# Performance work log

Hardware: AMD Instinct MI355X
Metric: run time of the kernel (lower is better)

The kernel has to match this reference:

```python
import jax, jax.numpy as jnp
import numpy as np

EPS = 1e-5
HEADS = 4
T_FRAMES, N_IND = 7, 12


def _bn(x, g, b):
    # training-mode BatchNorm1d over all nodes, per channel (biased variance)
    m = x.mean((0, 1))
    v = x.var((0, 1))
    return (x - m) * jax.lax.rsqrt(v + EPS) * g + b


def _gps_stack(h, gw, gb, qw, qb, ow, ob, bng, bnb, w1, b1, w2, b2):
    # h: [G, n, D]; params stacked over L layers on leading axis
    G, n, D = h.shape
    dh = D // HEADS
    inv_sqrt_dh = 1.0 / float(np.sqrt(dh))

    def layer(h, p):
        gw, gb, qw, qb, ow, ob, bng, bnb, w1, b1, w2, b2 = p
        # GCNConv on fully-connected graph (+self-loops): uniform 1/n aggregation
        xw = h @ gw.T + gb
        gcn = jnp.broadcast_to(xw.mean(axis=1, keepdims=True), h.shape)
        h1 = _bn(gcn + h, bng[0], bnb[0])
        # dense multi-head self-attention over each small graph
        qkv = h @ qw.T + qb                                   # [G, n, 3D]
        q, k, v = jnp.split(qkv, 3, axis=-1)
        q = q.reshape(G, n, HEADS, dh)
        k = k.reshape(G, n, HEADS, dh)
        v = v.reshape(G, n, HEADS, dh)
        scores = jnp.einsum('gqhd,gkhd->ghqk', q, k) * inv_sqrt_dh
        a = jax.nn.softmax(scores, axis=-1)
        attn = jnp.einsum('ghqk,gkhd->gqhd', a, v).reshape(G, n, D) @ ow.T + ob
        h2 = _bn(attn + h, bng[1], bnb[1])
        out = h1 + h2
        mlp = jax.nn.relu(out @ w1.T + b1) @ w2.T + b2
        out = _bn(out + mlp, bng[2], bnb[2])
        return out, None

    h, _ = jax.lax.scan(layer, h, (gw, gb, qw, qb, ow, ob, bng, bnb, w1, b1, w2, b2))
    return h


def setup_inputs() -> dict:
    key = jax.random.key(0)
    ks = jax.random.split(key, 8)
    B, J, D, L, C = 256, 17, 128, 3, 8

    def nrm(k, shape, s=0.05):
        return jax.random.normal(k, shape, dtype=jnp.float32) * s

    def layer_params(kbase):
        k = jax.random.split(kbase, 6)
        return dict(
            gw=nrm(k[0], (L, D, D)), gb=jnp.zeros((L, D), jnp.float32),
            qw=nrm(k[1], (L, 3 * D, D)), qb=jnp.zeros((L, 3 * D), jnp.float32),
            ow=nrm(k[2], (L, D, D)), ob=jnp.zeros((L, D), jnp.float32),
            bng=jnp.ones((L, 3, D), jnp.float32), bnb=jnp.zeros((L, 3, D), jnp.float32),
            w1=nrm(k[3], (L, 2 * D, D)), b1=jnp.zeros((L, 2 * D), jnp.float32),
            w2=nrm(k[4], (L, D, 2 * D)), b2=jnp.zeros((L, D), jnp.float32),
        )

    jp = layer_params(ks[0])
    ip = layer_params(ks[1])
    inp = {
        'poses': jax.random.normal(ks[2], (B, T_FRAMES * N_IND, J, 2), dtype=jnp.float32),
        'emb_w': nrm(ks[3], (D, 2), 0.5), 'emb_b': jnp.zeros((D,), jnp.float32),
        'cls_w': nrm(ks[4], (C, D), 0.1), 'cls_b': jnp.zeros((C,), jnp.float32),
    }
    for pfx, p in (('j_', jp), ('i_', ip)):
        for name, v in p.items():
            inp[pfx + name] = v
    return inp


def reference(poses, emb_w, emb_b, cls_w, cls_b,
              j_gw, j_gb, j_qw, j_qb, j_ow, j_ob, j_bng, j_bnb, j_w1, j_b1, j_w2, j_b2,
              i_gw, i_gb, i_qw, i_qb, i_ow, i_ob, i_bng, i_bnb, i_w1, i_b1, i_w2, i_b2):
    B, TN, J, _ = poses.shape
    T, N = T_FRAMES, N_IND
    D = emb_w.shape[0]
    # joint embedding: Linear(2, D) + LeakyReLU(0.01)
    h = jax.nn.leaky_relu(poses @ emb_w.T + emb_b, negative_slope=0.01)   # [B, TN, J, D]
    h = h.reshape(B * TN, J, D)
    h = _gps_stack(h, j_gw, j_gb, j_qw, j_qb, j_ow, j_ob, j_bng, j_bnb, j_w1, j_b1, j_w2, j_b2)
    h = h.reshape(B, T, N, J, D)
    ind = h.mean(axis=3)                                                  # [B, T, N, D]
    gi = ind.reshape(B * T, N, D)
    gi = _gps_stack(gi, i_gw, i_gb, i_qw, i_qb, i_ow, i_ob, i_bng, i_bnb, i_w1, i_b1, i_w2, i_b2)
    pooled = gi.reshape(B, T, N, D).mean(axis=(1, 2))                     # [B, D]
    return pooled @ cls_w.T + cls_b                                       # [B, 8]
```

## Files before the change

### kernel.cpp

```cpp
#include <hip/hip_runtime.h>
#include <hip/hip_bf16.h>

#define TID threadIdx.x

typedef __hip_bfloat16 bf16;
typedef short s8v __attribute__((ext_vector_type(8)));
typedef float f4v __attribute__((ext_vector_type(4)));
typedef float f16v __attribute__((ext_vector_type(16)));

__device__ __forceinline__ float b2f(bf16 x) { return __bfloat162float(x); }
__device__ __forceinline__ bf16  f2b(float x) { return __float2bfloat16(x); }
__device__ __forceinline__ short f2s(float x) {
    __hip_bfloat16 b = __float2bfloat16(x); short s; __builtin_memcpy(&s, &b, 2); return s;
}
__device__ __forceinline__ float bfu(short s) {
    unsigned u = ((unsigned)(unsigned short)s) << 16; float f; __builtin_memcpy(&f, &u, 4); return f;
}

#define B_   256
#define T_   7
#define NI_  12
#define TN_  84
#define J_   17
#define D_   128
#define H_   4
#define DH_  32
#define C_   8
#define G1_  21504
#define R1_  365568
#define G2_  1792
#define R2_  21504
#define EPS_ 1e-5f
#define NSLOT 32

__global__ __launch_bounds__(256)
void zero_kernel(float* __restrict__ p, int n)
{
    int stride = gridDim.x * 256;
    for (int i = blockIdx.x * 256 + TID; i < n; i += stride) p[i] = 0.f;
}

__global__ __launch_bounds__(128)
void setid_kernel(float* __restrict__ ab)
{
    ab[TID] = 1.f; ab[128 + TID] = 0.f;
}

__global__ __launch_bounds__(256)
void wconv_kernel(const float* __restrict__ src, bf16* __restrict__ dst, int n)
{
    int stride = gridDim.x * 256;
    for (int i = blockIdx.x * 256 + TID; i < n; i += stride) dst[i] = f2b(src[i]);
}

__global__ __launch_bounds__(256)
void embedv_kernel(const float* __restrict__ poses, const float* __restrict__ ew,
                   const float* __restrict__ eb, bf16* __restrict__ h, int R)
{
    __shared__ float sE0[128], sE1[128], sEb[128];
    if (TID < 128) { sE0[TID] = ew[2 * TID]; sE1[TID] = ew[2 * TID + 1]; sEb[TID] = eb[TID]; }
    __syncthreads();
    int stride = gridDim.x * 256;
    for (int i8 = blockIdx.x * 256 + TID; i8 < R * 16; i8 += stride) {
        int r = i8 >> 4, c8 = (i8 & 15) * 8;
        float p0 = poses[2 * r], p1 = poses[2 * r + 1];
        s8v o;
        #pragma unroll
        for (int e = 0; e < 8; ++e) {
            int c = c8 + e;
            float v = p0 * sE0[c] + p1 * sE1[c] + sEb[c];
            o[e] = f2s(v > 0.f ? v : 0.01f * v);
        }
        *(s8v*)(h + (size_t)r * D_ + c8) = o;
    }
}

__global__ __launch_bounds__(256)
void gmeanv_kernel(const bf16* __restrict__ h, const float* __restrict__ ab,
                   bf16* __restrict__ hbar, int G, int n)
{
    int i8 = blockIdx.x * 256 + TID;
    if (i8 >= G * 16) return;
    int g = i8 >> 4, c8 = (i8 & 15) * 8;
    const bf16* p = h + (size_t)g * n * D_ + c8;
    float acc[8] = {0,0,0,0,0,0,0,0};
    for (int j = 0; j < n; ++j) {
        s8v v = *(const s8v*)(p + j * D_);
        #pragma unroll
        for (int e = 0; e < 8; ++e) acc[e] += bfu(v[e]);
    }
    float rn = 1.f / n;
    s8v o;
    #pragma unroll
    for (int e = 0; e < 8; ++e) {
        int c = c8 + e;
        o[e] = f2s(acc[e] * rn * ab[c] + ab[128 + c]);
    }
    *(s8v*)(hbar + (size_t)g * D_ + c8) = o;
}

__global__ __launch_bounds__(256)
void linear64_kernel(const bf16* __restrict__ X, const bf16* __restrict__ Wb,
                     const float* __restrict__ bias, bf16* __restrict__ out)
{
    const int l = TID & 63, wid = TID >> 6;
    const size_t rbase = (size_t)blockIdx.x * 64;
    const int t = wid;
    const int arow = t * 16 + (l & 15);
    s8v a[4];
    #pragma unroll
    for (int ks = 0; ks < 4; ++ks)
        a[ks] = *(const s8v*)(X + (rbase + arow) * D_ + ks * 32 + ((l >> 4) * 8));
    for (int nt = 0; nt < 8; ++nt) {
        int col = nt * 16 + (l & 15);
        float bs = bias[col];
        f4v acc = {bs, bs, bs, bs};
        #pragma unroll
        for (int ks = 0; ks < 4; ++ks) {
            s8v b = *(const s8v*)(Wb + (size_t)col * D_ + ks * 32 + ((l >> 4) * 8));
            acc = __builtin_amdgcn_mfma_f32_16x16x32_bf16(a[ks], b, acc, 0, 0, 0);
        }
        #pragma unroll
        for (int r = 0; r < 4; ++r) {
            int row = t * 16 + (l >> 4) * 4 + r;
            out[(rbase + row) * D_ + col] = f2b(acc[r]);
        }
    }
}

template<int NN, int NG>
__global__ __launch_bounds__(256)
void attn_mfma_kernel(const bf16* __restrict__ h, const float* __restrict__ ab3,
                      const bf16* __restrict__ gcn,
                      const bf16* __restrict__ qwb, const float* __restrict__ qb,
                      const bf16* __restrict__ owb, const float* __restrict__ ob,
                      bf16* __restrict__ out, float* __restrict__ spart)
{
    constexpr int ROWS = NG * NN;
    constexpr int MT = (ROWS + 15) / 16;
    constexpr int QP = 3 * D_ + 24;
    constexpr int HP = 152;
    constexpr int NPAIR = NG * H_;
    __shared__ __align__(16) short sQKV[MT * 16][QP];
    __shared__ __align__(16) short sHN[ROWS][HP];
    __shared__ short sGCN[NG][128];
    __shared__ float sAB[256];
    __shared__ float sRED[512];

    const int l = TID & 63, wid = TID >> 6;
    const size_t gbase = (size_t)blockIdx.x * ROWS * D_;
    const bf16* hb = h + gbase;

    sAB[TID] = ab3[TID];
    for (int i = TID; i < NG * 128; i += 256)
        sGCN[i >> 7][i & 127] = ((const short*)gcn)[(size_t)blockIdx.x * NG * 128 + i];
    for (int i = TID; i < 512; i += 256) sRED[i] = 0.f;
    __syncthreads();

    for (int task = TID; task < ROWS * 16; task += 256) {
        int row = task >> 4, c8 = (task & 15) * 8;
        s8v raw = *(const s8v*)(hb + (size_t)row * D_ + c8);
        s8v af;
        #pragma unroll
        for (int e = 0; e < 8; ++e) {
            int c = c8 + e;
            af[e] = f2s(bfu(raw[e]) * sAB[c] + sAB[128 + c]);
        }
        *(s8v*)(&sHN[row][c8]) = af;
    }
    __syncthreads();

    s8v a[MT][4];
    #pragma unroll
    for (int t = 0; t < MT; ++t) {
        int row = t * 16 + (l & 15);
        if (row >= ROWS) row = ROWS - 1;
        const short* rp = &sHN[row][(l >> 4) * 8];
        #pragma unroll
        for (int ks = 0; ks < 4; ++ks) a[t][ks] = *(const s8v*)(rp + ks * 32);
    }
    for (int nt = wid; nt < 24; nt += 4) {
        int col = nt * 16 + (l & 15);
        const bf16* wp = qwb + (size_t)col * D_ + ((l >> 4) * 8);
        s8v b[4];
        #pragma unroll
        for (int ks = 0; ks < 4; ++ks) b[ks] = *(const s8v*)(wp + ks * 32);
        float bs = qb[col];
        #pragma unroll
        for (int t = 0; t < MT; ++t) {
            f4v acc = {bs, bs, bs, bs};
            #pragma unroll
            for (int ks = 0; ks < 4; ++ks)
                acc = __builtin_amdgcn_mfma_f32_16x16x32_bf16(a[t][ks], b[ks], acc, 0, 0, 0);
            #pragma unroll
            for (int r = 0; r < 4; ++r)
                sQKV[t * 16 + (l >> 4) * 4 + r][col] = f2s(acc[r]);
        }
    }
    __syncthreads();

    {
        const float inv = 0.17677669529663687f;
        const int l31 = l & 31, Gq = l >> 5;
        #pragma unroll
        for (int q = 0; q < NPAIR / 4; ++q) {
            int p = wid + 4 * q;
            int g = p >> 2, hd = p & 3;
            int gr = g * NN;
            int rr = gr + (l31 < NN ? l31 : NN - 1);
            s8v ka0 = *(const s8v*)(&sQKV[rr][D_ + hd * DH_ + Gq * 8]);
            s8v ka1 = *(const s8v*)(&sQKV[rr][D_ + hd * DH_ + Gq * 8 + 16]);
            s8v qb0 = *(const s8v*)(&sQKV[rr][hd * DH_ + Gq * 8]);
            s8v qb1 = *(const s8v*)(&sQKV[rr][hd * DH_ + Gq * 8 + 16]);
            f16v s = {};
            s = __builtin_amdgcn_mfma_f32_32x32x16_bf16(ka0, qb0, s, 0, 0, 0);
            s = __builtin_amdgcn_mfma_f32_32x32x16_bf16(ka1, qb1, s, 0, 0, 0);
            float m = -1e30f;
            #pragma unroll
            for (int r = 0; r < 16; ++r) {
                int j = (r & 3) + 8 * (r >> 2) + 4 * Gq;
                if (j < NN) m = fmaxf(m, s[r]);
            }
            m = fmaxf(m, __shfl_xor(m, 32));
            float pv[16]; float sum = 0.f;
            #pragma unroll
            for (int r = 0; r < 16; ++r) {
                int j = (r & 3) + 8 * (r >> 2) + 4 * Gq;
                float e = (j < NN) ? __expf((s[r] - m) * inv) : 0.f;
                pv[r] = e; sum += e;
            }
            sum += __shfl_xor(sum, 32);
            float rs = 1.f / sum;
            if (l31 < NN) {
                #pragma unroll
                for (int r = 0; r < 16; ++r) {
                    int j = (r & 3) + 8 * (r >> 2) + 4 * Gq;
                    sQKV[gr + l31][D_ + hd * DH_ + j] = f2s(pv[r] * rs);
                }
            }
            int prow = gr + l31; if (prow > MT * 16 - 1) prow = MT * 16 - 1;
            s8v pa0 = *(const s8v*)(&sQKV[prow][D_ + hd * DH_ + Gq * 8]);
            s8v pa1 = *(const s8v*)(&sQKV[prow][D_ + hd * DH_ + Gq * 8 + 16]);
            s8v vb0, vb1;
            #pragma unroll
            for (int e = 0; e < 8; ++e) {
                int j0 = Gq * 8 + e;      int jj0 = j0 < NN ? j0 : 0;
                int j1 = 16 + Gq * 8 + e; int jj1 = j1 < NN ? j1 : 0;
                vb0[e] = sQKV[gr + jj0][2 * D_ + hd * DH_ + l31];
                vb1[e] = sQKV[gr + jj1][2 * D_ + hd * DH_ + l31];
            }
            f16v o = {};
            o = __builtin_amdgcn_mfma_f32_32x32x16_bf16(pa0, vb0, o, 0, 0, 0);
            o = __builtin_amdgcn_mfma_f32_32x32x16_bf16(pa1, vb1, o, 0, 0, 0);
            #pragma unroll
            for (int r = 0; r < 16; ++r) {
                int i = (r & 3) + 8 * (r >> 2) + 4 * Gq;
                if (i < NN) sQKV[gr + i][hd * DH_ + l31] = f2s(o[r]);
            }
        }
    }
    __syncthreads();

    bf16* og = out + gbase;
    #pragma unroll
    for (int t = 0; t < MT; ++t) {
        int row = t * 16 + (l & 15);
        if (row >= ROWS) row = ROWS - 1;
        const short* rp = &sQKV[row][(l >> 4) * 8];
        #pragma unroll
        for (int ks = 0; ks < 4; ++ks) a[t][ks] = *(const s8v*)(rp + ks * 32);
    }
    #pragma unroll
    for (int ni = 0; ni < 2; ++ni) {
        int nt = wid + 4 * ni;
        int col = nt * 16 + (l & 15);
        const bf16* wp = owb + (size_t)col * D_ + ((l >> 4) * 8);
        s8v b[4];
        #pragma unroll
        for (int ks = 0; ks < 4; ++ks) b[ks] = *(const s8v*)(wp + ks * 32);
        float bs = ob[col];
        float s1 = 0.f, q1 = 0.f, s2 = 0.f, q2 = 0.f;
        #pragma unroll
        for (int t = 0; t < MT; ++t) {
            f4v acc = {bs, bs, bs, bs};
            #pragma unroll
            for (int ks = 0; ks < 4; ++ks)
                acc = __builtin_amdgcn_mfma_f32_16x16x32_bf16(a[t][ks], b[ks], acc, 0, 0, 0);
            #pragma unroll
            for (int r = 0; r < 4; ++r) {
                int row = t * 16 + (l >> 4) * 4 + r;
                if (row < ROWS) {
                    float res = bfu(sHN[row][col]);
                    float t2v = acc[r] + res;
                    og[(size_t)row * D_ + col] = f2b(t2v);
                    s2 += t2v; q2 += t2v * t2v;
                    int g = row / NN;
                    float x1 = res + bfu(sGCN[g][col]);
                    s1 += x1; q1 += x1 * x1;
                }
            }
        }
        atomicAdd(&sRED[col], s1);
        atomicAdd(&sRED[128 + col], q1);
        atomicAdd(&sRED[256 + col], s2);
        atomicAdd(&sRED[384 + col], q2);
    }
    __syncthreads();
    {
        int slot = blockIdx.x & (NSLOT - 1);
        for (int i = TID; i < 512; i += 256) atomicAdd(&spart[slot * 512 + i], sRED[i]);
    }
}

__global__ __launch_bounds__(128)
void finalize12_kernel(float* __restrict__ spart, const float* __restrict__ bng,
                       const float* __restrict__ bnb, float rcount,
                       float* __restrict__ ab12)
{
    int c = TID;
    float s1 = 0, q1 = 0, s2 = 0, q2 = 0;
    for (int s = 0; s < NSLOT; ++s) {
        float* p = spart + s * 512;
        s1 += p[c]; q1 += p[128 + c]; s2 += p[256 + c]; q2 += p[384 + c];
        p[c] = 0.f; p[128 + c] = 0.f; p[256 + c] = 0.f; p[384 + c] = 0.f;
    }
    float m1 = s1 * rcount, v1 = q1 * rcount - m1 * m1;
    float a1 = rsqrtf(v1 + EPS_) * bng[c];
    ab12[c] = a1; ab12[128 + c] = bnb[c] - m1 * a1;
    float m2 = s2 * rcount, v2 = q2 * rcount - m2 * m2;
    float a2 = rsqrtf(v2 + EPS_) * bng[128 + c];
    ab12[256 + c] = a2; ab12[384 + c] = bnb[128 + c] - m2 * a2;
}

__global__ __launch_bounds__(128)
void finalize3_kernel(float* __restrict__ spart, const float* __restrict__ gamma,
                      const float* __restrict__ beta, float rcount,
                      float* __restrict__ ab3)
{
    int c = TID;
    float s1 = 0, q1 = 0;
    for (int s = 0; s < NSLOT; ++s) {
        float* p = spart + s * 256;
        s1 += p[c]; q1 += p[128 + c];
        p[c] = 0.f; p[128 + c] = 0.f;
    }
    float m = s1 * rcount, v = q1 * rcount - m * m;
    float a = rsqrtf(v + EPS_) * gamma[c];
    ab3[c] = a; ab3[128 + c] = beta[c] - m * a;
}

__global__ __launch_bounds__(256)
void mlp_mfma_kernel(bf16* __restrict__ X, const float* __restrict__ ab3,
                     const bf16* __restrict__ gcn, const bf16* __restrict__ t2,
                     const float* __restrict__ ab12,
                     const bf16* __restrict__ w1b, const float* __restrict__ b1,
                     const bf16* __restrict__ w2b, const float* __restrict__ b2,
                     int n, float* __restrict__ spart3)
{
    constexpr int MP = 264;
    __shared__ short sM[64][MP];
    __shared__ short sOUT[64][136];
    __shared__ float sAB[768];
    __shared__ float sRED[256];
    const int l = TID & 63, wid = TID >> 6;
    const size_t rbase = (size_t)blockIdx.x * 64;
    bf16* Xb = X + rbase * D_;
    const bf16* Tb = t2 + rbase * D_;

    sAB[TID] = ab3[TID];
    for (int i = TID; i < 512; i += 256) sAB[256 + i] = ab12[i];
    sRED[TID] = 0.f;
    __syncthreads();

    {
        int row = TID >> 2;
        int cb0 = (TID & 3) * 32;
        int g = (int)((rbase + row) / n);
        #pragma unroll
        for (int k2 = 0; k2 < 4; ++k2) {
            int cb = cb0 + k2 * 8;
            s8v xv = *(const s8v*)(Xb + (size_t)row * D_ + cb);
            s8v gv = *(const s8v*)(gcn + (size_t)g * D_ + cb);
            s8v tv = *(const s8v*)(Tb + (size_t)row * D_ + cb);
            s8v af;
            #pragma unroll
            for (int e = 0; e < 8; ++e) {
                int c = cb + e;
                float hn = bfu(xv[e]) * sAB[c] + sAB[128 + c];
                float outv = (hn + bfu(gv[e])) * sAB[256 + c] + sAB[384 + c]
                           + bfu(tv[e]) * sAB[512 + c] + sAB[640 + c];
                af[e] = f2s(outv);
            }
            *(s8v*)(&sOUT[row][cb]) = af;
        }
    }
    __syncthreads();

    s8v a[4][4];
    #pragma unroll
    for (int t = 0; t < 4; ++t) {
        const short* rp = &sOUT[t * 16 + (l & 15)][(l >> 4) * 8];
        #pragma unroll
        for (int ks = 0; ks < 4; ++ks) a[t][ks] = *(const s8v*)(rp + ks * 32);
    }
    for (int nt = wid; nt < 16; nt += 4) {
        int col = nt * 16 + (l & 15);
        const bf16* wp = w1b + (size_t)col * D_ + ((l >> 4) * 8);
        s8v b[4];
        #pragma unroll
        for (int ks = 0; ks < 4; ++ks) b[ks] = *(const s8v*)(wp + ks * 32);
        float bs = b1[col];
        #pragma unroll
        for (int t = 0; t < 4; ++t) {
            f4v acc = {bs, bs, bs, bs};
            #pragma unroll
            for (int ks = 0; ks < 4; ++ks)
                acc = __builtin_amdgcn_mfma_f32_16x16x32_bf16(a[t][ks], b[ks], acc, 0, 0, 0);
            #pragma unroll
            for (int r = 0; r < 4; ++r)
                sM[t * 16 + (l >> 4) * 4 + r][col] = f2s(fmaxf(acc[r], 0.f));
        }
    }
    __syncthreads();

    {
        const int nt0 = wid * 2;
        const int col0 = nt0 * 16 + (l & 15), col1 = col0 + 16;
        s8v b0[8], b1v[8];
        #pragma unroll
        for (int ks = 0; ks < 8; ++ks) {
            b0[ks]  = *(const s8v*)(w2b + (size_t)col0 * 256 + ks * 32 + ((l >> 4) * 8));
            b1v[ks] = *(const s8v*)(w2b + (size_t)col1 * 256 + ks * 32 + ((l >> 4) * 8));
        }
        float bs0 = b2[col0], bs1 = b2[col1];
        float ss0 = 0.f, qq0 = 0.f, ss1 = 0.f, qq1 = 0.f;
        #pragma unroll
        for (int t = 0; t < 4; ++t) {
            s8v am[8];
            const short* rp = &sM[t * 16 + (l & 15)][(l >> 4) * 8];
            #pragma unroll
            for (int ks = 0; ks < 8; ++ks) am[ks] = *(const s8v*)(rp + ks * 32);
            f4v acc0 = {bs0, bs0, bs0, bs0};
            f4v acc1 = {bs1, bs1, bs1, bs1};
            #pragma unroll
            for (int ks = 0; ks < 8; ++ks) {
                acc0 = __builtin_amdgcn_mfma_f32_16x16x32_bf16(am[ks], b0[ks], acc0, 0, 0, 0);
                acc1 = __builtin_amdgcn_mfma_f32_16x16x32_bf16(am[ks], b1v[ks], acc1, 0, 0, 0);
            }
            #pragma unroll
            for (int r = 0; r < 4; ++r) {
                int row = t * 16 + (l >> 4) * 4 + r;
                float xn0 = acc0[r] + bfu(sOUT[row][col0]);
                float xn1 = acc1[r] + bfu(sOUT[row][col1]);
                Xb[(size_t)row * D_ + col0] = f2b(xn0);
                Xb[(size_t)row * D_ + col1] = f2b(xn1);
                ss0 += xn0; qq0 += xn0 * xn0;
                ss1 += xn1; qq1 += xn1 * xn1;
            }
        }
        atomicAdd(&sRED[col0], ss0); atomicAdd(&sRED[128 + col0], qq0);
        atomicAdd(&sRED[col1], ss1); atomicAdd(&sRED[128 + col1], qq1);
    }
    __syncthreads();
    {
        int slot = blockIdx.x & (NSLOT - 1);
        atomicAdd(&spart3[slot * 256 + TID], sRED[TID]);
    }
}

__global__ __launch_bounds__(128)
void poolcls_kernel(const bf16* __restrict__ gi, const float* __restrict__ ab,
                    const float* __restrict__ cw, const float* __restrict__ cb,
                    float* __restrict__ out)
{
    __shared__ float sP[128];
    int b = blockIdx.x, d = TID;
    const bf16* p = gi + (size_t)b * TN_ * D_ + d;
    float s = 0.f;
    for (int i = 0; i < TN_; ++i) s += b2f(p[i * D_]);
    sP[d] = (s * (1.f / TN_)) * ab[d] + ab[128 + d];
    __syncthreads();
    if (d < C_) {
        float acc = cb[d];
        for (int k = 0; k < D_; ++k) acc += sP[k] * cw[d * D_ + k];
        out[b * C_ + d] = acc;
    }
}

extern "C" void kernel_launch(void* const* d_in, const int* in_sizes, int n_in,
                              void* d_out, int out_size, void* d_ws, size_t ws_size,
                              hipStream_t stream)
{
    (void)in_sizes; (void)n_in; (void)out_size; (void)ws_size;

    const float* poses = (const float*)d_in[0];
    const float* emb_w = (const float*)d_in[1];
    const float* emb_b = (const float*)d_in[2];
    const float* cls_w = (const float*)d_in[3];
    const float* cls_b = (const float*)d_in[4];
    const float* jp[12]; const float* ip[12];
    for (int k = 0; k < 12; ++k) { jp[k] = (const float*)d_in[5 + k]; ip[k] = (const float*)d_in[17 + k]; }

    char* base = (char*)d_ws;
    size_t off = 0;
    auto alloc_b = [&](size_t elems) -> bf16* {
        bf16* p = (bf16*)(base + off);
        off = (off + elems * sizeof(bf16) + 255) & ~(size_t)255;
        return p;
    };
    bf16* bufA  = alloc_b((size_t)R1_ * D_);
    bf16* bufB  = alloc_b((size_t)R1_ * D_);
    bf16* hbarJ = alloc_b((size_t)G1_ * D_);
    bf16* gcn1  = alloc_b((size_t)G1_ * D_);
    bf16* hbar2 = alloc_b((size_t)G2_ * D_);
    bf16* gcn2  = alloc_b((size_t)G2_ * D_);
    float* spart12 = (float*)(base + off); off += NSLOT * 512 * 4;
    float* spart3  = (float*)(base + off); off += NSLOT * 256 * 4;
    float* ab3     = (float*)(base + off); off += 256 * 4;
    float* ab12    = (float*)(base + off); off = (off + 512 * 4 + 255) & ~(size_t)255;
    bf16* wb[2][5];
    const int wsz[5] = {3 * D_ * D_, 3 * 3 * D_ * D_, 3 * D_ * D_, 3 * 2 * D_ * D_, 3 * 2 * D_ * D_};
    for (int s = 0; s < 2; ++s)
        for (int k = 0; k < 5; ++k) wb[s][k] = alloc_b((size_t)wsz[k]);

    const int widx[5] = {0, 2, 4, 8, 10};
    for (int s = 0; s < 2; ++s) {
        const float** P = s ? ip : jp;
        for (int k = 0; k < 5; ++k)
            wconv_kernel<<<(wsz[k] + 4095) / 4096, 256, 0, stream>>>(P[widx[k]], wb[s][k], wsz[k]);
    }
    zero_kernel<<<24, 256, 0, stream>>>(spart12, NSLOT * 512 + NSLOT * 256);

    embedv_kernel<<<4096, 256, 0, stream>>>(poses, emb_w, emb_b, bufA, R1_);

    auto run_stage = [&](const float** P, const bf16* const* W, bf16* h, bf16* t2,
                         bf16* hbar, bf16* gcn, int G, int n, int R) {
        setid_kernel<<<1, 128, 0, stream>>>(ab3);
        for (int L = 0; L < 3; ++L) {
            const bf16* gwb = W[0] + (size_t)L * D_ * D_;
            const bf16* qwb = W[1] + (size_t)L * 3 * D_ * D_;
            const bf16* owb = W[2] + (size_t)L * D_ * D_;
            const bf16* w1b = W[3] + (size_t)L * 2 * D_ * D_;
            const bf16* w2b = W[4] + (size_t)L * 2 * D_ * D_;
            const float* gb  = P[1] + (size_t)L * D_;
            const float* qb  = P[3] + (size_t)L * 3 * D_;
            const float* ob  = P[5] + (size_t)L * D_;
            const float* bng = P[6] + (size_t)L * 3 * D_;
            const float* bnb = P[7] + (size_t)L * 3 * D_;
            const float* b1  = P[9] + (size_t)L * 2 * D_;
            const float* b2  = P[11] + (size_t)L * D_;
            float rcount = 1.f / (float)R;

            gmeanv_kernel<<<G * 16 / 256, 256, 0, stream>>>(h, ab3, hbar, G, n);
            linear64_kernel<<<G / 64, 256, 0, stream>>>(hbar, gwb, gb, gcn);
            if (n == J_)
                attn_mfma_kernel<J_, 2><<<G / 2, 256, 0, stream>>>(h, ab3, gcn, qwb, qb, owb, ob, t2, spart12);
            else
                attn_mfma_kernel<NI_, 4><<<G / 4, 256, 0, stream>>>(h, ab3, gcn, qwb, qb, owb, ob, t2, spart12);
            finalize12_kernel<<<1, 128, 0, stream>>>(spart12, bng, bnb, rcount, ab12);
            mlp_mfma_kernel<<<R / 64, 256, 0, stream>>>(h, ab3, gcn, t2, ab12,
                                                        w1b, b1, w2b, b2, n, spart3);
            finalize3_kernel<<<1, 128, 0, stream>>>(spart3, bng + 2 * D_, bnb + 2 * D_,
                                                    rcount, ab3);
        }
    };

    run_stage(jp, wb[0], bufA, bufB, hbarJ, gcn1, G1_, J_, R1_);
    gmeanv_kernel<<<G1_ * 16 / 256, 256, 0, stream>>>(bufA, ab3, hbarJ, G1_, J_);
    run_stage(ip, wb[1], hbarJ, bufB, hbar2, gcn2, G2_, NI_, R2_);
    poolcls_kernel<<<B_, 128, 0, stream>>>(hbarJ, ab3, cls_w, cls_b, (float*)d_out);
}
```

Measured before the change: 1.689 ms.

## Fuse GCN mean and linear into attention kernel; use wave-shuffle BN stat reduction

The per-graph mean and the GCN linear projection are now computed inside the attention kernel from the already-normalized rows held in shared memory. This removes two kernel launches per layer and a global round trip for hbar and gcn. The GCN result is still written out for the MLP kernel. BatchNorm partial sums in the attention and MLP kernels are now reduced with wave shuffles and sent directly to global atomics, replacing the shared-memory atomic staging. The tradeoff is more global atomics per block and an extra serial mean computation inside attention. The mean is taken from bf16-rounded normalized values, which may slightly change precision.

```diff
diff --git a/kernel.cpp b/kernel.cpp
--- a/kernel.cpp
+++ b/kernel.cpp
@@ -99,42 +99,14 @@
     *(s8v*)(hbar + (size_t)g * D_ + c8) = o;
 }
 
-__global__ __launch_bounds__(256)
-void linear64_kernel(const bf16* __restrict__ X, const bf16* __restrict__ Wb,
-                     const float* __restrict__ bias, bf16* __restrict__ out)
-{
-    const int l = TID & 63, wid = TID >> 6;
-    const size_t rbase = (size_t)blockIdx.x * 64;
-    const int t = wid;
-    const int arow = t * 16 + (l & 15);
-    s8v a[4];
-    #pragma unroll
-    for (int ks = 0; ks < 4; ++ks)
-        a[ks] = *(const s8v*)(X + (rbase + arow) * D_ + ks * 32 + ((l >> 4) * 8));
-    for (int nt = 0; nt < 8; ++nt) {
-        int col = nt * 16 + (l & 15);
-        float bs = bias[col];
-        f4v acc = {bs, bs, bs, bs};
-        #pragma unroll
-        for (int ks = 0; ks < 4; ++ks) {
-            s8v b = *(const s8v*)(Wb + (size_t)col * D_ + ks * 32 + ((l >> 4) * 8));
-            acc = __builtin_amdgcn_mfma_f32_16x16x32_bf16(a[ks], b, acc, 0, 0, 0);
-        }
-        #pragma unroll
-        for (int r = 0; r < 4; ++r) {
-            int row = t * 16 + (l >> 4) * 4 + r;
-            out[(rbase + row) * D_ + col] = f2b(acc[r]);
-        }
-    }
-}
-
 template<int NN, int NG>
 __global__ __launch_bounds__(256)
 void attn_mfma_kernel(const bf16* __restrict__ h, const float* __restrict__ ab3,
-                      const bf16* __restrict__ gcn,
+                      const bf16* __restrict__ gwb, const float* __restrict__ gb,
                       const bf16* __restrict__ qwb, const float* __restrict__ qb,
                       const bf16* __restrict__ owb, const float* __restrict__ ob,
-                      bf16* __restrict__ out, float* __restrict__ spart)
+                      bf16* __restrict__ out, bf16* __restrict__ gcnb,
+                      float* __restrict__ spart)
 {
     constexpr int ROWS = NG * NN;
     constexpr int MT = (ROWS + 15) / 16;
@@ -143,18 +115,15 @@
     constexpr int NPAIR = NG * H_;
     __shared__ __align__(16) short sQKV[MT * 16][QP];
     __shared__ __align__(16) short sHN[ROWS][HP];
+    __shared__ __align__(16) short sHB[NG][128];
     __shared__ short sGCN[NG][128];
     __shared__ float sAB[256];
-    __shared__ float sRED[512];
 
     const int l = TID & 63, wid = TID >> 6;
     const size_t gbase = (size_t)blockIdx.x * ROWS * D_;
     const bf16* hb = h + gbase;
 
     sAB[TID] = ab3[TID];
-    for (int i = TID; i < NG * 128; i += 256)
-        sGCN[i >> 7][i & 127] = ((const short*)gcn)[(size_t)blockIdx.x * NG * 128 + i];
-    for (int i = TID; i < 512; i += 256) sRED[i] = 0.f;
     __syncthreads();
 
     for (int task = TID; task < ROWS * 16; task += 256) {
@@ -179,6 +148,42 @@
         #pragma unroll
         for (int ks = 0; ks < 4; ++ks) a[t][ks] = *(const s8v*)(rp + ks * 32);
     }
+
+    for (int task = TID; task < NG * D_; task += 256) {
+        int g = task >> 7, col = task & 127;
+        float s = 0.f;
+        for (int j = 0; j < NN; ++j) s += bfu(sHN[g * NN + j][col]);
+        sHB[g][col] = f2s(s * (1.f / NN));
+    }
+    __syncthreads();
+
+    {
+        int rclamp = (l & 15) < NG ? (l & 15) : NG - 1;
+        s8v ag[4];
+        #pragma unroll
+        for (int ks = 0; ks < 4; ++ks)
+            ag[ks] = *(const s8v*)(&sHB[rclamp][ks * 32 + ((l >> 4) * 8)]);
+        bf16* gout = gcnb + (size_t)blockIdx.x * NG * D_;
+        #pragma unroll
+        for (int ci = 0; ci < 2; ++ci) {
+            int col = (wid * 2 + ci) * 16 + (l & 15);
+            float bs = gb[col];
+            f4v acc = {bs, bs, bs, bs};
+            #pragma unroll
+            for (int ks = 0; ks < 4; ++ks) {
+                s8v b = *(const s8v*)(gwb + (size_t)col * D_ + ks * 32 + ((l >> 4) * 8));
+                acc = __builtin_amdgcn_mfma_f32_16x16x32_bf16(ag[ks], b, acc, 0, 0, 0);
+            }
+            if ((l >> 4) == 0) {
+                #pragma unroll
+                for (int r = 0; r < NG; ++r) {
+                    sGCN[r][col] = f2s(acc[r]);
+                    gout[(size_t)r * D_ + col] = f2b(acc[r]);
+                }
+            }
+        }
+    }
+
     for (int nt = wid; nt < 24; nt += 4) {
         int col = nt * 16 + (l & 15);
         const bf16* wp = qwb + (size_t)col * D_ + ((l >> 4) * 8);
@@ -270,6 +275,7 @@
         #pragma unroll
         for (int ks = 0; ks < 4; ++ks) a[t][ks] = *(const s8v*)(rp + ks * 32);
     }
+    const int slot = blockIdx.x & (NSLOT - 1);
     #pragma unroll
     for (int ni = 0; ni < 2; ++ni) {
         int nt = wid + 4 * ni;
@@ -300,15 +306,16 @@
                 }
             }
         }
-        atomicAdd(&sRED[col], s1);
-        atomicAdd(&sRED[128 + col], q1);
-        atomicAdd(&sRED[256 + col], s2);
-        atomicAdd(&sRED[384 + col], q2);
-    }
-    __syncthreads();
-    {
-        int slot = blockIdx.x & (NSLOT - 1);
-        for (int i = TID; i < 512; i += 256) atomicAdd(&spart[slot * 512 + i], sRED[i]);
+        s1 += __shfl_xor(s1, 16); s1 += __shfl_xor(s1, 32);
+        q1 += __shfl_xor(q1, 16); q1 += __shfl_xor(q1, 32);
+        s2 += __shfl_xor(s2, 16); s2 += __shfl_xor(s2, 32);
+        q2 += __shfl_xor(q2, 16); q2 += __shfl_xor(q2, 32);
+        if ((l >> 4) == 0) {
+            atomicAdd(&spart[slot * 512 + col], s1);
+            atomicAdd(&spart[slot * 512 + 128 + col], q1);
+            atomicAdd(&spart[slot * 512 + 256 + col], s2);
+            atomicAdd(&spart[slot * 512 + 384 + col], q2);
+        }
     }
 }
 
@@ -361,7 +368,6 @@
     __shared__ short sM[64][MP];
     __shared__ short sOUT[64][136];
     __shared__ float sAB[768];
-    __shared__ float sRED[256];
     const int l = TID & 63, wid = TID >> 6;
     const size_t rbase = (size_t)blockIdx.x * 64;
     bf16* Xb = X + rbase * D_;
@@ -369,7 +375,6 @@
 
     sAB[TID] = ab3[TID];
     for (int i = TID; i < 512; i += 256) sAB[256 + i] = ab12[i];
-    sRED[TID] = 0.f;
     __syncthreads();
 
     {
@@ -458,13 +463,17 @@
                 ss1 += xn1; qq1 += xn1 * xn1;
             }
         }
-        atomicAdd(&sRED[col0], ss0); atomicAdd(&sRED[128 + col0], qq0);
-        atomicAdd(&sRED[col1], ss1); atomicAdd(&sRED[128 + col1], qq1);
-    }
-    __syncthreads();
-    {
-        int slot = blockIdx.x & (NSLOT - 1);
-        atomicAdd(&spart3[slot * 256 + TID], sRED[TID]);
+        ss0 += __shfl_xor(ss0, 16); ss0 += __shfl_xor(ss0, 32);
+        qq0 += __shfl_xor(qq0, 16); qq0 += __shfl_xor(qq0, 32);
+        ss1 += __shfl_xor(ss1, 16); ss1 += __shfl_xor(ss1, 32);
+        qq1 += __shfl_xor(qq1, 16); qq1 += __shfl_xor(qq1, 32);
+        if ((l >> 4) == 0) {
+            int slot = blockIdx.x & (NSLOT - 1);
+            atomicAdd(&spart3[slot * 256 + col0], ss0);
+            atomicAdd(&spart3[slot * 256 + 128 + col0], qq0);
+            atomicAdd(&spart3[slot * 256 + col1], ss1);
+            atomicAdd(&spart3[slot * 256 + 128 + col1], qq1);
+        }
     }
 }
 
@@ -512,7 +521,6 @@
     bf16* bufB  = alloc_b((size_t)R1_ * D_);
     bf16* hbarJ = alloc_b((size_t)G1_ * D_);
     bf16* gcn1  = alloc_b((size_t)G1_ * D_);
-    bf16* hbar2 = alloc_b((size_t)G2_ * D_);
     bf16* gcn2  = alloc_b((size_t)G2_ * D_);
     float* spart12 = (float*)(base + off); off += NSLOT * 512 * 4;
     float* spart3  = (float*)(base + off); off += NSLOT * 256 * 4;
@@ -534,7 +542,7 @@
     embedv_kernel<<<4096, 256, 0, stream>>>(poses, emb_w, emb_b, bufA, R1_);
 
     auto run_stage = [&](const float** P, const bf16* const* W, bf16* h, bf16* t2,
-                         bf16* hbar, bf16* gcn, int G, int n, int R) {
+                         bf16* gcn, int G, int n, int R) {
         setid_kernel<<<1, 128, 0, stream>>>(ab3);
         for (int L = 0; L < 3; ++L) {
             const bf16* gwb = W[0] + (size_t)L * D_ * D_;
@@ -551,12 +559,12 @@
             const float* b2  = P[11] + (size_t)L * D_;
             float rcount = 1.f / (float)R;
 
-            gmeanv_kernel<<<G * 16 / 256, 256, 0, stream>>>(h, ab3, hbar, G, n);
-            linear64_kernel<<<G / 64, 256, 0, stream>>>(hbar, gwb, gb, gcn);
             if (n == J_)
-                attn_mfma_kernel<J_, 2><<<G / 2, 256, 0, stream>>>(h, ab3, gcn, qwb, qb, owb, ob, t2, spart12);
+                attn_mfma_kernel<J_, 2><<<G / 2, 256, 0, stream>>>(
+                    h, ab3, gwb, gb, qwb, qb, owb, ob, t2, gcn, spart12);
             else
-                attn_mfma_kernel<NI_, 4><<<G / 4, 256, 0, stream>>>(h, ab3, gcn, qwb, qb, owb, ob, t2, spart12);
+                attn_mfma_kernel<NI_, 4><<<G / 4, 256, 0, stream>>>(
+                    h, ab3, gwb, gb, qwb, qb, owb, ob, t2, gcn, spart12);
             finalize12_kernel<<<1, 128, 0, stream>>>(spart12, bng, bnb, rcount, ab12);
             mlp_mfma_kernel<<<R / 64, 256, 0, stream>>>(h, ab3, gcn, t2, ab12,
                                                         w1b, b1, w2b, b2, n, spart3);
@@ -565,8 +573,8 @@
         }
     };
 
-    run_stage(jp, wb[0], bufA, bufB, hbarJ, gcn1, G1_, J_, R1_);
+    run_stage(jp, wb[0], bufA, bufB, gcn1, G1_, J_, R1_);
     gmeanv_kernel<<<G1_ * 16 / 256, 256, 0, stream>>>(bufA, ab3, hbarJ, G1_, J_);
-    run_stage(ip, wb[1], hbarJ, bufB, hbar2, gcn2, G2_, NI_, R2_);
+    run_stage(ip, wb[1], hbarJ, bufB, gcn2, G2_, NI_, R2_);
     poolcls_kernel<<<B_, 128, 0, stream>>>(hbarJ, ab3, cls_w, cls_b, (float*)d_out);
 }
```

New measurement: 1.429 ms. -15.4%, faster.
